# Performance work log

Measured on AMD Instinct MI355X. Metric: run time of the kernel, lower is better.

Reference implementation:

```python
import jax, jax.numpy as jnp
import numpy as np

MARGIN = 0.0625  # init kwarg `margin`; barrier = relu


def setup_inputs() -> dict:
    key = jax.random.key(0)
    k1, k2, k3, k4 = jax.random.split(key, 4)
    B, N, M = 64, 64, 100000
    return {
        "outputs": jax.random.normal(k1, (B, N, 3), dtype=jnp.float32),
        "c2ws": jax.random.normal(k2, (B, 4, 4), dtype=jnp.float32),
        "scene_scales": jax.random.uniform(k3, (B,), dtype=jnp.float32),
        "means": jax.random.normal(k4, (M, 3), dtype=jnp.float32),
    }


def reference(outputs, c2ws, scene_scales, means):
    # aff = R * s (per-batch scaled rotation block), trans = translation column
    aff = c2ws[:, :3, :3] * scene_scales[:, None, None]      # [B,3,3]
    trans = c2ws[:, :3, 3]                                   # [B,3]
    # retrajs = baddbmm(trans, outputs, aff.mT) = outputs @ aff^T + trans
    retrajs = jnp.einsum("bnj,bij->bni", outputs, aff) + trans[:, None, :]
    q = retrajs.reshape(-1, 3)                               # [Q,3], Q = B*N
    # Brute-force nearest neighbor (replaces kd_tree.query); torch_kdtree
    # returns SQUARED euclidean distances, so we keep d^2.
    # d2[q,m] = |q|^2 + |m|^2 - 2 q.m  -> [Q,M] (the dominant memory-bound op)
    d2 = (
        jnp.sum(q * q, axis=-1, keepdims=True)
        + jnp.sum(means * means, axis=-1)[None, :]
        - 2.0 * (q @ means.T)
    )
    dists = jnp.maximum(jnp.min(d2, axis=1), 0.0)            # [Q]
    loss = jnp.mean(jax.nn.relu(-(dists - MARGIN)))
    return loss
```

## Files before the change

kernel.cpp:

```cpp
#include <hip/hip_runtime.h>

#define MARGIN 0.0625f

#define P 4096
#define M 100000
#define G 500
#define CHUNK 200
#define NQUAD (CHUNK / 4)
#define QS 4
#define R 4
#define NCOPY 32

typedef float float2v __attribute__((ext_vector_type(2)));
typedef float float4v __attribute__((ext_vector_type(4)));

#define WS_PMIN_OFF 0

static __device__ __forceinline__ float2v pk_fma(float2v a, float2v b, float2v c) {
    float2v d;
    asm("v_pk_fma_f32 %0, %1, %2, %3" : "=v"(d) : "v"(a), "v"(b), "v"(c));
    return d;
}
static __device__ __forceinline__ float min3f(float a, float b, float c) {
    float d;
    asm("v_min3_f32 %0, %1, %2, %3" : "=v"(d) : "v"(a), "v"(b), "v"(c));
    return d;
}

__global__ __launch_bounds__(256, 4) void nn_kernel(
    const float* __restrict__ outputs,
    const float* __restrict__ c2ws,
    const float* __restrict__ scales,
    const float* __restrict__ means,
    unsigned int* __restrict__ pmin)
{
    const int t  = threadIdx.x;
    const int g  = blockIdx.x;
    const int qs = blockIdx.y;
    const int pbase = qs * (P / QS);
    const int mbase = g * CHUNK;

    __shared__ float4v lxs[NQUAD], lys[NQUAD], lzs[NQUAD], lms[NQUAD];

    if (t < CHUNK) {
        const float* mp = means + 3 * (mbase + t);
        float x = mp[0], y = mp[1], z = mp[2];
        ((float*)lxs)[t] = -2.0f * x;
        ((float*)lys)[t] = -2.0f * y;
        ((float*)lzs)[t] = -2.0f * z;
        ((float*)lms)[t] = fmaf(x, x, fmaf(y, y, z * z));
    }

    float2v qxs[R], qys[R], qzs[R];
    float qq[R], mnlo[R], mnhi[R];
#pragma unroll
    for (int i = 0; i < R; ++i) {
        int p = pbase + i * 256 + t;
        int b = p >> 6;
        float s  = scales[b];
        float o0 = outputs[3 * p + 0];
        float o1 = outputs[3 * p + 1];
        float o2 = outputs[3 * p + 2];
        const float* cw = c2ws + b * 16;
        float q0 = fmaf(s, fmaf(cw[0],  o0, fmaf(cw[1],  o1, cw[2]  * o2)), cw[3]);
        float q1 = fmaf(s, fmaf(cw[4],  o0, fmaf(cw[5],  o1, cw[6]  * o2)), cw[7]);
        float q2 = fmaf(s, fmaf(cw[8],  o0, fmaf(cw[9],  o1, cw[10] * o2)), cw[11]);
        qq[i]  = fmaf(q0, q0, fmaf(q1, q1, q2 * q2));
        qxs[i] = (float2v){q0, q0};
        qys[i] = (float2v){q1, q1};
        qzs[i] = (float2v){q2, q2};
        mnlo[i] = 1e30f;
        mnhi[i] = 1e30f;
    }

    __syncthreads();

    float4v cx = lxs[0], cy = lys[0], cz = lzs[0], cm = lms[0];
#pragma unroll 2
    for (int j = 0; j < NQUAD; ++j) {
        int jn = (j + 1 < NQUAD) ? j + 1 : 0;
        float4v nx = lxs[jn], ny = lys[jn], nz = lzs[jn], nm = lms[jn];

        float2v cx0 = __builtin_shufflevector(cx, cx, 0, 1);
        float2v cx1 = __builtin_shufflevector(cx, cx, 2, 3);
        float2v cy0 = __builtin_shufflevector(cy, cy, 0, 1);
        float2v cy1 = __builtin_shufflevector(cy, cy, 2, 3);
        float2v cz0 = __builtin_shufflevector(cz, cz, 0, 1);
        float2v cz1 = __builtin_shufflevector(cz, cz, 2, 3);
        float2v cm0 = __builtin_shufflevector(cm, cm, 0, 1);
        float2v cm1 = __builtin_shufflevector(cm, cm, 2, 3);
#pragma unroll
        for (int i = 0; i < R; ++i) {
            float2v t0 = pk_fma(qxs[i], cx0, cm0);
            t0 = pk_fma(qys[i], cy0, t0);
            t0 = pk_fma(qzs[i], cz0, t0);
            float2v t1 = pk_fma(qxs[i], cx1, cm1);
            t1 = pk_fma(qys[i], cy1, t1);
            t1 = pk_fma(qzs[i], cz1, t1);
            mnlo[i] = min3f(t0[0], t1[0], mnlo[i]);
            mnhi[i] = min3f(t0[1], t1[1], mnhi[i]);
        }
        cx = nx; cy = ny; cz = nz; cm = nm;
    }

    unsigned int* __restrict__ pm = pmin + (g & (NCOPY - 1)) * P;
#pragma unroll
    for (int i = 0; i < R; ++i) {
        int p = pbase + i * 256 + t;
        float m = fminf(mnlo[i], mnhi[i]);
        float d = fmaxf(qq[i] + m, 0.0f);
        unsigned int bits = __float_as_uint(d);
        if (bits < pm[p]) atomicMin(&pm[p], bits);
    }
}

__global__ __launch_bounds__(256) void finish_kernel(
    const unsigned int* __restrict__ pmin,
    float* __restrict__ out)
{
    const int t = threadIdx.x;
    const int q = blockIdx.x * 256 + t;

    unsigned int mb = 0xFFFFFFFFu;
#pragma unroll
    for (int c = 0; c < NCOPY; ++c)
        mb = min(mb, pmin[c * P + q]);

    float m = __uint_as_float(mb);
    float v = fmaxf(MARGIN - m, 0.0f) * (1.0f / (float)P);

#pragma unroll
    for (int off = 32; off > 0; off >>= 1)
        v += __shfl_down(v, off, 64);

    __shared__ float lds[4];
    int wid = t >> 6;
    if ((t & 63) == 0) lds[wid] = v;
    __syncthreads();
    if (t == 0)
        atomicAdd(out, lds[0] + lds[1] + lds[2] + lds[3]);
}

extern "C" void kernel_launch(void* const* d_in, const int* in_sizes, int n_in,
                              void* d_out, int out_size, void* d_ws, size_t ws_size,
                              hipStream_t stream) {
    const float* outputs = (const float*)d_in[0];
    const float* c2ws    = (const float*)d_in[1];
    const float* scales  = (const float*)d_in[2];
    const float* means   = (const float*)d_in[3];

    unsigned int* pmin = (unsigned int*)((char*)d_ws + WS_PMIN_OFF);
    float* out = (float*)d_out;

    hipMemsetAsync(pmin, 0xFF, NCOPY * P * sizeof(unsigned int), stream);
    hipMemsetAsync(out, 0, sizeof(float), stream);

    nn_kernel<<<dim3(G, QS), 256, 0, stream>>>(outputs, c2ws, scales, means, pmin);
    finish_kernel<<<P / 256, 256, 0, stream>>>(pmin, out);
}
```

Baseline: 100.7 us.

## Process two means chunks per block with prefetch; replace packed FMA with scalar FMA

Each block now handles two 200-point chunks of means. The second chunk's coordinates are loaded from global memory into registers before the first scan and written to a second LDS buffer after it. This halves the grid and amortizes query setup and the atomic writes across twice the work. The inner loop also drops v_pk_fma_f32 in favour of scalar fmaf with a single min accumulator per query. That may change ALU throughput and adds a second __syncthreads per block.

```diff
diff --git a/kernel.cpp b/kernel.cpp
--- a/kernel.cpp
+++ b/kernel.cpp
@@ -9,18 +9,14 @@
 #define NQUAD (CHUNK / 4)
 #define QS 4
 #define R 4
+#define NCH 2
+#define GB (G / NCH)
 #define NCOPY 32
 
-typedef float float2v __attribute__((ext_vector_type(2)));
 typedef float float4v __attribute__((ext_vector_type(4)));
 
 #define WS_PMIN_OFF 0
 
-static __device__ __forceinline__ float2v pk_fma(float2v a, float2v b, float2v c) {
-    float2v d;
-    asm("v_pk_fma_f32 %0, %1, %2, %3" : "=v"(d) : "v"(a), "v"(b), "v"(c));
-    return d;
-}
 static __device__ __forceinline__ float min3f(float a, float b, float c) {
     float d;
     asm("v_min3_f32 %0, %1, %2, %3" : "=v"(d) : "v"(a), "v"(b), "v"(c));
@@ -35,24 +31,23 @@
     unsigned int* __restrict__ pmin)
 {
     const int t  = threadIdx.x;
-    const int g  = blockIdx.x;
+    const int gb = blockIdx.x;
     const int qs = blockIdx.y;
     const int pbase = qs * (P / QS);
-    const int mbase = g * CHUNK;
+    const int mbase = gb * NCH * CHUNK;
 
-    __shared__ float4v lxs[NQUAD], lys[NQUAD], lzs[NQUAD], lms[NQUAD];
+    __shared__ float4v lxs[2][NQUAD], lys[2][NQUAD], lzs[2][NQUAD], lms[2][NQUAD];
 
     if (t < CHUNK) {
         const float* mp = means + 3 * (mbase + t);
         float x = mp[0], y = mp[1], z = mp[2];
-        ((float*)lxs)[t] = -2.0f * x;
-        ((float*)lys)[t] = -2.0f * y;
-        ((float*)lzs)[t] = -2.0f * z;
-        ((float*)lms)[t] = fmaf(x, x, fmaf(y, y, z * z));
+        ((float*)lxs[0])[t] = -2.0f * x;
+        ((float*)lys[0])[t] = -2.0f * y;
+        ((float*)lzs[0])[t] = -2.0f * z;
+        ((float*)lms[0])[t] = fmaf(x, x, fmaf(y, y, z * z));
     }
 
-    float2v qxs[R], qys[R], qzs[R];
-    float qq[R], mnlo[R], mnhi[R];
+    float q0[R], q1[R], q2[R], qq[R], mn[R];
 #pragma unroll
     for (int i = 0; i < R; ++i) {
         int p = pbase + i * 256 + t;
@@ -62,53 +57,64 @@
         float o1 = outputs[3 * p + 1];
         float o2 = outputs[3 * p + 2];
         const float* cw = c2ws + b * 16;
-        float q0 = fmaf(s, fmaf(cw[0],  o0, fmaf(cw[1],  o1, cw[2]  * o2)), cw[3]);
-        float q1 = fmaf(s, fmaf(cw[4],  o0, fmaf(cw[5],  o1, cw[6]  * o2)), cw[7]);
-        float q2 = fmaf(s, fmaf(cw[8],  o0, fmaf(cw[9],  o1, cw[10] * o2)), cw[11]);
-        qq[i]  = fmaf(q0, q0, fmaf(q1, q1, q2 * q2));
-        qxs[i] = (float2v){q0, q0};
-        qys[i] = (float2v){q1, q1};
-        qzs[i] = (float2v){q2, q2};
-        mnlo[i] = 1e30f;
-        mnhi[i] = 1e30f;
+        q0[i] = fmaf(s, fmaf(cw[0],  o0, fmaf(cw[1],  o1, cw[2]  * o2)), cw[3]);
+        q1[i] = fmaf(s, fmaf(cw[4],  o0, fmaf(cw[5],  o1, cw[6]  * o2)), cw[7]);
+        q2[i] = fmaf(s, fmaf(cw[8],  o0, fmaf(cw[9],  o1, cw[10] * o2)), cw[11]);
+        qq[i] = fmaf(q0[i], q0[i], fmaf(q1[i], q1[i], q2[i] * q2[i]));
+        mn[i] = 1e30f;
     }
 
     __syncthreads();
 
-    float4v cx = lxs[0], cy = lys[0], cz = lzs[0], cm = lms[0];
-#pragma unroll 2
-    for (int j = 0; j < NQUAD; ++j) {
-        int jn = (j + 1 < NQUAD) ? j + 1 : 0;
-        float4v nx = lxs[jn], ny = lys[jn], nz = lzs[jn], nm = lms[jn];
-
-        float2v cx0 = __builtin_shufflevector(cx, cx, 0, 1);
-        float2v cx1 = __builtin_shufflevector(cx, cx, 2, 3);
-        float2v cy0 = __builtin_shufflevector(cy, cy, 0, 1);
-        float2v cy1 = __builtin_shufflevector(cy, cy, 2, 3);
-        float2v cz0 = __builtin_shufflevector(cz, cz, 0, 1);
-        float2v cz1 = __builtin_shufflevector(cz, cz, 2, 3);
-        float2v cm0 = __builtin_shufflevector(cm, cm, 0, 1);
-        float2v cm1 = __builtin_shufflevector(cm, cm, 2, 3);
-#pragma unroll
-        for (int i = 0; i < R; ++i) {
-            float2v t0 = pk_fma(qxs[i], cx0, cm0);
-            t0 = pk_fma(qys[i], cy0, t0);
-            t0 = pk_fma(qzs[i], cz0, t0);
-            float2v t1 = pk_fma(qxs[i], cx1, cm1);
-            t1 = pk_fma(qys[i], cy1, t1);
-            t1 = pk_fma(qzs[i], cz1, t1);
-            mnlo[i] = min3f(t0[0], t1[0], mnlo[i]);
-            mnhi[i] = min3f(t0[1], t1[1], mnhi[i]);
-        }
-        cx = nx; cy = ny; cz = nz; cm = nm;
+    float nx_ = 0.0f, ny_ = 0.0f, nz_ = 0.0f;
+    if (t < CHUNK) {
+        const float* mp = means + 3 * (mbase + CHUNK + t);
+        nx_ = mp[0]; ny_ = mp[1]; nz_ = mp[2];
     }
 
-    unsigned int* __restrict__ pm = pmin + (g & (NCOPY - 1)) * P;
+#define SCAN(b)                                                               \
+    do {                                                                      \
+        float4v cx = lxs[b][0], cy = lys[b][0], cz = lzs[b][0], cm = lms[b][0];\
+        _Pragma("unroll 2")                                                   \
+        for (int j = 0; j < NQUAD; ++j) {                                     \
+            int jn = (j + 1 < NQUAD) ? j + 1 : 0;                             \
+            float4v nx = lxs[b][jn], ny = lys[b][jn],                         \
+                    nz = lzs[b][jn], nm = lms[b][jn];                         \
+            _Pragma("unroll")                                                 \
+            for (int i = 0; i < R; ++i) {                                     \
+                float t0 = fmaf(q2[i], cz[0], fmaf(q1[i], cy[0],              \
+                           fmaf(q0[i], cx[0], cm[0])));                       \
+                float t1 = fmaf(q2[i], cz[1], fmaf(q1[i], cy[1],              \
+                           fmaf(q0[i], cx[1], cm[1])));                       \
+                float t2 = fmaf(q2[i], cz[2], fmaf(q1[i], cy[2],              \
+                           fmaf(q0[i], cx[2], cm[2])));                       \
+                float t3 = fmaf(q2[i], cz[3], fmaf(q1[i], cy[3],              \
+                           fmaf(q0[i], cx[3], cm[3])));                       \
+                mn[i] = min3f(t0, t1, mn[i]);                                 \
+                mn[i] = min3f(t2, t3, mn[i]);                                 \
+            }                                                                 \
+            cx = nx; cy = ny; cz = nz; cm = nm;                               \
+        }                                                                     \
+    } while (0)
+
+    SCAN(0);
+
+    if (t < CHUNK) {
+        ((float*)lxs[1])[t] = -2.0f * nx_;
+        ((float*)lys[1])[t] = -2.0f * ny_;
+        ((float*)lzs[1])[t] = -2.0f * nz_;
+        ((float*)lms[1])[t] = fmaf(nx_, nx_, fmaf(ny_, ny_, nz_ * nz_));
+    }
+    __syncthreads();
+
+    SCAN(1);
+#undef SCAN
+
+    unsigned int* __restrict__ pm = pmin + (gb & (NCOPY - 1)) * P;
 #pragma unroll
     for (int i = 0; i < R; ++i) {
         int p = pbase + i * 256 + t;
-        float m = fminf(mnlo[i], mnhi[i]);
-        float d = fmaxf(qq[i] + m, 0.0f);
+        float d = fmaxf(qq[i] + mn[i], 0.0f);
         unsigned int bits = __float_as_uint(d);
         if (bits < pm[p]) atomicMin(&pm[p], bits);
     }
@@ -155,6 +161,6 @@
     hipMemsetAsync(pmin, 0xFF, NCOPY * P * sizeof(unsigned int), stream);
     hipMemsetAsync(out, 0, sizeof(float), stream);
 
-    nn_kernel<<<dim3(G, QS), 256, 0, stream>>>(outputs, c2ws, scales, means, pmin);
+    nn_kernel<<<dim3(GB, QS), 256, 0, stream>>>(outputs, c2ws, scales, means, pmin);
     finish_kernel<<<P / 256, 256, 0, stream>>>(pmin, out);
 }
```

Measured after the change: 102.4 us. About the same (+1.7%).
